# Kernel optimization log

Measured on AMD Instinct MI355X. Metric: run time of the kernel, lower is better.

Reference implementation:

```python
import math
import jax, jax.numpy as jnp
import numpy as np

N, L, C_IMG, D, FF, H, NL, V = 2, 1024, 512, 512, 2048, 8, 4, 8000
EPS_ATTN = 1e-6
EPS_LN = 1e-5


def pos_enc(position, channels):
    # position: (N, L, 1) float. channels assumed even here (256 / 512).
    num = channels // 2
    log_inc = math.log(10000.0) / (num - 1)
    inv = jnp.exp(jnp.arange(num, dtype=position.dtype) * -log_inc)
    st = position * inv.reshape(1, 1, -1)  # (N, L, num)
    return jnp.concatenate([jnp.sin(st), jnp.cos(st)], -1)


def layer_norm(x, s, b):
    m = jnp.mean(x, -1, keepdims=True)
    v = jnp.mean((x - m) ** 2, -1, keepdims=True)
    return (x - m) / jnp.sqrt(v + EPS_LN) * s + b


def causal_linear_attention(x, mask, Wq, bq, Wk, bk, Wv, bv, Wo, bo):
    # x: (N, L, D), mask: (N, L, 1)
    n, l, d = x.shape
    q = (x @ Wq + bq).reshape(n, l, H, -1)
    k = (x @ Wk + bk).reshape(n, l, H, -1)
    v = (x @ Wv + bv).reshape(n, l, H, -1)
    Q = jax.nn.elu(q) + 1.0                       # elu feature map
    K = (jax.nn.elu(k) + 1.0) * mask[:, :, :, None]
    K_cum = jnp.cumsum(K, axis=1)                 # (N, L, H, dk)
    Z = 1.0 / (jnp.einsum('nlhd,nlhd->nlh', Q, K_cum) + EPS_ATTN)
    KV = jnp.cumsum(K[..., :, None] * v[..., None, :], axis=1)  # (N, L, H, dk, dv)
    out = jnp.einsum('nlhd,nlhde->nlhe', Q, KV) * Z[..., None]
    return out.reshape(n, l, d) @ Wo + bo


def encoder_layer(x, mask, p):
    (Wq, bq, Wk, bk, Wv, bv, Wo, bo, W1, b1, W2, b2, s1, be1, s2, be2) = p
    x = x + causal_linear_attention(x, mask, Wq, bq, Wk, bk, Wv, bv, Wo, bo)
    x = layer_norm(x, s1, be1)
    y = jax.nn.gelu(x @ W1 + b1, approximate=False) @ W2 + b2
    return layer_norm(x + y, s2, be2)


def setup_inputs() -> dict:
    key = jax.random.key(0)
    ks = iter(jax.random.split(key, 64))

    def p(shape):
        return jax.random.normal(next(ks), shape, dtype=jnp.float32) * 0.02

    x_img = jax.random.normal(next(ks), (N, L, C_IMG), dtype=jnp.float32)
    x_txt = jax.random.randint(next(ks), (N, L), 0, V)
    pos = jnp.broadcast_to(jnp.arange(L, dtype=jnp.float32)[None, :, None], (N, L, 1))
    pos_r = jnp.floor(pos / 32.0)
    pos_c = jnp.mod(pos, 32.0)
    pos_t = pos
    first_half = (jnp.arange(L) < L // 2).astype(jnp.float32)[None, :, None]
    mask_img = jnp.broadcast_to(first_half, (N, L, 1))
    mask_txt = 1.0 - mask_img

    inp = dict(x_img=x_img, x_txt=x_txt, mask_img=mask_img, mask_txt=mask_txt,
               pos_r=pos_r, pos_c=pos_c, pos_t=pos_t,
               W_ei=p((C_IMG, D)), b_ei=jnp.zeros((D,)),
               emb_txt=p((V, D)),
               Wq=p((NL, D, D)), bq=jnp.zeros((NL, D)),
               Wk=p((NL, D, D)), bk=jnp.zeros((NL, D)),
               Wv=p((NL, D, D)), bv=jnp.zeros((NL, D)),
               Wo=p((NL, D, D)), bo=jnp.zeros((NL, D)),
               W1=p((NL, D, FF)), b1=jnp.zeros((NL, FF)),
               W2=p((NL, FF, D)), b2=jnp.zeros((NL, D)),
               ln1_s=jnp.ones((NL, D)), ln1_b=jnp.zeros((NL, D)),
               ln2_s=jnp.ones((NL, D)), ln2_b=jnp.zeros((NL, D)),
               W_pi=p((D, C_IMG)), b_pi=jnp.zeros((C_IMG,)),
               W_pt=p((D, V)), b_pt=jnp.zeros((V,)))
    return inp


def reference(x_img, x_txt, mask_img, mask_txt, pos_r, pos_c, pos_t,
              W_ei, b_ei, emb_txt,
              Wq, bq, Wk, bk, Wv, bv, Wo, bo, W1, b1, W2, b2,
              ln1_s, ln1_b, ln2_s, ln2_b, W_pi, b_pi, W_pt, b_pt):
    x_mask = mask_img + mask_txt  # (N, L, 1)
    # image embedding
    half = D // 2
    x_pos = jnp.concatenate([pos_enc(pos_r, half), pos_enc(pos_c, D - half)], -1)
    x_emb_img = ((x_img @ W_ei + b_ei) + x_pos) * mask_img
    # text embedding
    x_emb_txt = (emb_txt[x_txt] + pos_enc(pos_t, D)) * mask_txt
    x = x_emb_img + x_emb_txt
    for i in range(NL):
        p = (Wq[i], bq[i], Wk[i], bk[i], Wv[i], bv[i], Wo[i], bo[i],
             W1[i], b1[i], W2[i], b2[i], ln1_s[i], ln1_b[i], ln2_s[i], ln2_b[i])
        x = encoder_layer(x, x_mask, p)
    logit_img = x @ W_pi + b_pi
    logit_txt = x @ W_pt + b_pt
    return (logit_img, logit_txt)
```

## Files before the change

### kernel.cpp

```cpp
#include <hip/hip_runtime.h>
#include <hip/hip_bf16.h>
#include <math.h>

#define NB 2
#define LSEQ 1024
#define DM 512
#define FFD 2048
#define NHEAD 8
#define DKH 64
#define NLAYER 4
#define VOCAB 8000
#define NCHUNK 16
#define NROWS (NB * LSEQ)
#define QS 1536
#define NHEADCAT 8512
#define NHEADPAD 8576

#define OP_NONE 0
#define OP_GELU 2
#define OP_QKV  3
#define OP_PART 4
#define OP_HEAD 5

typedef __attribute__((ext_vector_type(8))) short short8;
typedef __attribute__((ext_vector_type(4))) float f32x4;
typedef __hip_bfloat16 bf16;

__device__ __forceinline__ void cast_tile(
    const float* __restrict__ s, bf16* __restrict__ d, int K, int N,
    int n0, int k0, int tx, int ty)
{
    __shared__ float tile[32][33];
    #pragma unroll
    for (int i = 0; i < 4; ++i) {
        const int k = k0 + ty + 8 * i;
        const int n = n0 + tx;
        tile[ty + 8 * i][tx] = (n < N) ? s[(size_t)k * N + n] : 0.f;
    }
    __syncthreads();
    #pragma unroll
    for (int i = 0; i < 4; ++i) {
        const int n = n0 + ty + 8 * i;
        d[(size_t)n * K + k0 + tx] = __float2bfloat16(tile[tx][ty + 8 * i]);
    }
}

__global__ __launch_bounds__(256) void cast_t(
    const float* __restrict__ src, bf16* __restrict__ dst,
    int K, int N, size_t sStride, size_t dStride)
{
    const int z = blockIdx.z;
    cast_tile(src + (size_t)z * sStride, dst + (size_t)z * dStride, K, N,
              blockIdx.x * 32, blockIdx.y * 32,
              threadIdx.x & 31, threadIdx.x >> 5);
}

__global__ __launch_bounds__(256) void cast_qkvo(
    const float* __restrict__ Wq, const float* __restrict__ Wk,
    const float* __restrict__ Wv, const float* __restrict__ Wo,
    bf16* __restrict__ QKVt, bf16* __restrict__ Wot)
{
    const int z = blockIdx.z, layer = z >> 2, which = z & 3;
    const float* src = (which == 0 ? Wq : which == 1 ? Wk : which == 2 ? Wv : Wo)
                       + (size_t)layer * 262144;
    bf16* dst = (which < 3) ? (QKVt + (size_t)layer * 786432 + (size_t)which * 262144)
                            : (Wot + (size_t)layer * 262144);
    cast_tile(src, dst, 512, 512, blockIdx.x * 32, blockIdx.y * 32,
              threadIdx.x & 31, threadIdx.x >> 5);
}

__global__ __launch_bounds__(256) void cast_e(
    const float* __restrict__ src, bf16* __restrict__ dst, int n4)
{
    const int i = blockIdx.x * 256 + threadIdx.x;
    if (i < n4) {
        const float4 v = *(const float4*)(src + (size_t)i * 4);
        dst[(size_t)i * 4 + 0] = __float2bfloat16(v.x);
        dst[(size_t)i * 4 + 1] = __float2bfloat16(v.y);
        dst[(size_t)i * 4 + 2] = __float2bfloat16(v.z);
        dst[(size_t)i * 4 + 3] = __float2bfloat16(v.w);
    }
}

__global__ __launch_bounds__(256) void qkv_bias_k(
    const float* __restrict__ bq, const float* __restrict__ bk,
    const float* __restrict__ bv, float* __restrict__ out)
{
    const int z = blockIdx.x;
    for (int j = threadIdx.x; j < QS; j += 256) {
        float v;
        if (j < 512)       v = bq[z * DM + j];
        else if (j < 1024) v = bk[z * DM + j - 512];
        else               v = bv[z * DM + j - 1024];
        out[z * QS + j] = v;
    }
}

__global__ __launch_bounds__(256) void head_bias_k(
    const float* __restrict__ bpi, const float* __restrict__ bpt,
    float* __restrict__ hb)
{
    const int j = blockIdx.x * 256 + threadIdx.x;
    if (j < NHEADPAD)
        hb[j] = (j < 512) ? bpi[j] : (j < NHEADCAT ? bpt[j - 512] : 0.f);
}

template<int BM, int BN>
__global__ __launch_bounds__(256) void gemm16(
    const bf16* __restrict__ A, const bf16* __restrict__ Bt,
    const float* __restrict__ bias, const float* __restrict__ res,
    float* __restrict__ outF, float* __restrict__ outF2,
    bf16* __restrict__ outH,
    int M, int K, int Nout, int op, int kslab)
{
    constexpr int WM = BM / 2, WN = BN / 2, MI = WM / 16, NI = WN / 16;
    __shared__ bf16 As[BM * 32];
    __shared__ bf16 Bs[BN * 32];
    const int tid = threadIdx.x;
    const int lane = tid & 63;
    const int wave = tid >> 6;
    const int wm = (wave >> 1) * WM, wn = (wave & 1) * WN;
    const int bm = blockIdx.y * BM, bn = blockIdx.x * BN;
    const int l16 = lane & 15, quad = lane >> 4;

    const int rA = tid >> 2;
    const int c8 = (tid & 3) << 3;

    f32x4 acc[MI][NI];
    #pragma unroll
    for (int i = 0; i < MI; ++i)
        #pragma unroll
        for (int j = 0; j < NI; ++j) acc[i][j] = (f32x4){0.f, 0.f, 0.f, 0.f};

    const bf16* gA = A  + (size_t)(bm + rA) * K + c8;
    const bf16* gB = Bt + (size_t)(bn + rA) * K + c8;
    const int ldsWaveOff = wave * 1024;

    const int kStart = blockIdx.z * kslab;
    for (int k0 = kStart; k0 < kStart + kslab; k0 += 32) {
        __syncthreads();
        #pragma unroll
        for (int i = 0; i < BM / 64; ++i)
            __builtin_amdgcn_global_load_lds(
                (const __attribute__((address_space(1))) void*)(gA + (size_t)i * 64 * K + k0),
                (__attribute__((address_space(3))) void*)((char*)As + i * 4096 + ldsWaveOff),
                16, 0, 0);
        #pragma unroll
        for (int i = 0; i < BN / 64; ++i)
            __builtin_amdgcn_global_load_lds(
                (const __attribute__((address_space(1))) void*)(gB + (size_t)i * 64 * K + k0),
                (__attribute__((address_space(3))) void*)((char*)Bs + i * 4096 + ldsWaveOff),
                16, 0, 0);
        __syncthreads();
        short8 a[MI], b[NI];
        #pragma unroll
        for (int i = 0; i < MI; ++i)
            a[i] = *(const short8*)(As + (size_t)(wm + i * 16 + l16) * 32 + quad * 8);
        #pragma unroll
        for (int j = 0; j < NI; ++j)
            b[j] = *(const short8*)(Bs + (size_t)(wn + j * 16 + l16) * 32 + quad * 8);
        #pragma unroll
        for (int i = 0; i < MI; ++i)
            #pragma unroll
            for (int j = 0; j < NI; ++j)
                acc[i][j] = __builtin_amdgcn_mfma_f32_16x16x32_bf16(
                    a[i], b[j], acc[i][j], 0, 0, 0);
    }

    if (op == OP_PART) {
        float* dst = outF + (size_t)blockIdx.z * (size_t)M * Nout;
        #pragma unroll
        for (int j = 0; j < NI; ++j) {
            const int col = bn + wn + j * 16 + l16;
            #pragma unroll
            for (int i = 0; i < MI; ++i)
                #pragma unroll
                for (int r = 0; r < 4; ++r) {
                    const int row = bm + wm + i * 16 + quad * 4 + r;
                    dst[(size_t)row * Nout + col] = acc[i][j][r];
                }
        }
        return;
    }
    if (op == OP_HEAD) {
        #pragma unroll
        for (int j = 0; j < NI; ++j) {
            const int col = bn + wn + j * 16 + l16;
            const bool cok = (col < NHEADCAT);
            const float bz = cok ? bias[col] : 0.f;
            #pragma unroll
            for (int i = 0; i < MI; ++i)
                #pragma unroll
                for (int r = 0; r < 4; ++r) {
                    const int row = bm + wm + i * 16 + quad * 4 + r;
                    const float v = acc[i][j][r] + bz;
                    if (cok) {
                        if (col < 512) outF[(size_t)row * 512 + col] = v;
                        else           outF2[(size_t)row * VOCAB + (col - 512)] = v;
                    }
                }
        }
        return;
    }

    #pragma unroll
    for (int j = 0; j < NI; ++j) {
        const int col = bn + wn + j * 16 + l16;
        const bool cok = (col < Nout);
        const float bz = cok ? bias[col] : 0.f;
        #pragma unroll
        for (int i = 0; i < MI; ++i) {
            #pragma unroll
            for (int r = 0; r < 4; ++r) {
                const int row = bm + wm + i * 16 + quad * 4 + r;
                float v = acc[i][j][r] + bz;
                if (op == OP_GELU)      v = 0.5f * v * (1.f + erff(v * 0.70710678118654752f));
                else if (op == OP_QKV && col < 1024) v = (v > 0.f) ? v + 1.f : expf(v);
                if (cok) {
                    if (res)  v += res[(size_t)row * Nout + col];
                    if (outF) outF[(size_t)row * Nout + col] = v;
                    if (outH) outH[(size_t)row * Nout + col] = __float2bfloat16(v);
                }
            }
        }
    }
}

__global__ __launch_bounds__(256) void embed_k(
    const float* __restrict__ gI, const int* __restrict__ xt,
    const float* __restrict__ emb,
    const float* __restrict__ mi, const float* __restrict__ mt,
    const float* __restrict__ pr, const float* __restrict__ pc,
    const float* __restrict__ pt, float* __restrict__ X, bf16* __restrict__ Xh)
{
    const int row = blockIdx.x;
    const float prv = pr[row], pcv = pc[row], ptv = pt[row];
    const float miv = mi[row], mtv = mt[row];
    const int tok = xt[row];
    const float LOG1E4 = 9.2103403719761836f;
    const float LI127 = LOG1E4 / 127.f;
    const float LI255 = LOG1E4 / 255.f;

    for (int d = threadIdx.x; d < DM; d += 256) {
        float ip;
        if (d < 128)       ip = sinf(prv * expf(-(float)d * LI127));
        else if (d < 256)  ip = cosf(prv * expf(-(float)(d - 128) * LI127));
        else if (d < 384)  ip = sinf(pcv * expf(-(float)(d - 256) * LI127));
        else               ip = cosf(pcv * expf(-(float)(d - 384) * LI127));
        float tp;
        if (d < 256) tp = sinf(ptv * expf(-(float)d * LI255));
        else         tp = cosf(ptv * expf(-(float)(d - 256) * LI255));
        const float v = miv * (gI[(size_t)row * DM + d] + ip)
                      + mtv * (emb[(size_t)tok * DM + d] + tp);
        X[(size_t)row * DM + d] = v;
        Xh[(size_t)row * DM + d] = __float2bfloat16(v);
    }
}

__global__ __launch_bounds__(256) void ln_red(
    const float* __restrict__ P, int nP,
    const float* __restrict__ bias, const float* __restrict__ res,
    const float* __restrict__ g, const float* __restrict__ b,
    float* __restrict__ out, bf16* __restrict__ outh)
{
    const int row = blockIdx.x;
    const int tid = threadIdx.x;
    const size_t base = (size_t)row * DM;
    float x0 = res[base + tid] + bias[tid];
    float x1 = res[base + tid + 256] + bias[tid + 256];
    for (int p = 0; p < nP; ++p) {
        x0 += P[(size_t)p * 1048576 + base + tid];
        x1 += P[(size_t)p * 1048576 + base + tid + 256];
    }
    __shared__ float red[256];
    red[tid] = x0 + x1;
    __syncthreads();
    for (int off = 128; off > 0; off >>= 1) {
        if (tid < off) red[tid] += red[tid + off];
        __syncthreads();
    }
    const float mean = red[0] / (float)DM;
    __syncthreads();
    const float d0 = x0 - mean, d1 = x1 - mean;
    red[tid] = d0 * d0 + d1 * d1;
    __syncthreads();
    for (int off = 128; off > 0; off >>= 1) {
        if (tid < off) red[tid] += red[tid + off];
        __syncthreads();
    }
    const float var = red[0] / (float)DM;
    const float rstd = rsqrtf(var + 1e-5f);
    const float y0 = d0 * rstd * g[tid] + b[tid];
    const float y1 = d1 * rstd * g[tid + 256] + b[tid + 256];
    out[base + tid]        = y0;
    out[base + tid + 256]  = y1;
    outh[base + tid]       = __float2bfloat16(y0);
    outh[base + tid + 256] = __float2bfloat16(y1);
}

__global__ __launch_bounds__(256) void attn_kv(
    const float* __restrict__ Kp, const float* __restrict__ Vp,
    float* __restrict__ S, float* __restrict__ ks)
{
    const int c = blockIdx.x, h = blockIdx.y, n = blockIdx.z;
    const int tid = threadIdx.x;
    __shared__ float sK[64][64], sV[64][64], part[4][64];

    const int lr = tid >> 4;
    const int c4 = (tid & 15) * 4;
    #pragma unroll
    for (int it = 0; it < 4; ++it) {
        const int row = it * 16 + lr;
        const size_t gb = ((size_t)(n * LSEQ + c * 64 + row)) * QS + h * DKH + c4;
        *(float4*)&sK[row][c4] = *(const float4*)(Kp + gb);
        *(float4*)&sV[row][c4] = *(const float4*)(Vp + gb);
    }
    __syncthreads();

    const int e = tid & 63, dq = tid >> 6;
    float s[16] = {};
    for (int l = 0; l < 64; ++l) {
        const float vv = sV[l][e];
        const float4 k0 = *(const float4*)&sK[l][dq * 16 + 0];
        const float4 k1 = *(const float4*)&sK[l][dq * 16 + 4];
        const float4 k2 = *(const float4*)&sK[l][dq * 16 + 8];
        const float4 k3 = *(const float4*)&sK[l][dq * 16 + 12];
        s[0]  = fmaf(k0.x, vv, s[0]);  s[1]  = fmaf(k0.y, vv, s[1]);
        s[2]  = fmaf(k0.z, vv, s[2]);  s[3]  = fmaf(k0.w, vv, s[3]);
        s[4]  = fmaf(k1.x, vv, s[4]);  s[5]  = fmaf(k1.y, vv, s[5]);
        s[6]  = fmaf(k1.z, vv, s[6]);  s[7]  = fmaf(k1.w, vv, s[7]);
        s[8]  = fmaf(k2.x, vv, s[8]);  s[9]  = fmaf(k2.y, vv, s[9]);
        s[10] = fmaf(k2.z, vv, s[10]); s[11] = fmaf(k2.w, vv, s[11]);
        s[12] = fmaf(k3.x, vv, s[12]); s[13] = fmaf(k3.y, vv, s[13]);
        s[14] = fmaf(k3.z, vv, s[14]); s[15] = fmaf(k3.w, vv, s[15]);
    }
    const size_t sb = (((size_t)(n * NHEAD + h)) * NCHUNK + c) * 4096;
    #pragma unroll
    for (int i = 0; i < 16; ++i) S[sb + (size_t)(dq * 16 + i) * 64 + e] = s[i];

    float kp = 0.f;
    #pragma unroll
    for (int i = 0; i < 16; ++i) kp += sK[dq * 16 + i][e];
    part[dq][e] = kp;
    __syncthreads();
    if (tid < 64)
        ks[(((size_t)(n * NHEAD + h)) * NCHUNK + c) * 64 + tid] =
            part[0][tid] + part[1][tid] + part[2][tid] + part[3][tid];
}

__global__ __launch_bounds__(256) void attn_prefix(
    float* __restrict__ S, float* __restrict__ ks)
{
    const int gid = blockIdx.x * 256 + threadIdx.x;
    const int nh = gid >> 12, j = gid & 4095;
    const size_t base = ((size_t)nh * NCHUNK) * 4096 + j;
    float run = 0.f;
    #pragma unroll
    for (int c = 0; c < NCHUNK; ++c) {
        const float t = S[base + (size_t)c * 4096];
        S[base + (size_t)c * 4096] = run;
        run += t;
    }
    if (gid < NB * NHEAD * 64) {
        const int nh2 = gid >> 6, j2 = gid & 63;
        const size_t kb = ((size_t)nh2 * NCHUNK) * 64 + j2;
        float kr = 0.f;
        #pragma unroll
        for (int c = 0; c < NCHUNK; ++c) {
            const float t = ks[kb + c * 64];
            ks[kb + c * 64] = kr;
            kr += t;
        }
    }
}

__global__ __launch_bounds__(256) void attn_out(
    const float* __restrict__ QKV, const float* __restrict__ S,
    const float* __restrict__ ks, bf16* __restrict__ O)
{
    const int c = blockIdx.x, h = blockIdx.y, n = blockIdx.z;
    const int tid = threadIdx.x;
    __shared__ float sQt[64][64];
    __shared__ float sKt[64][64];
    __shared__ float sV [64][64];
    __shared__ float sS [64][64];
    __shared__ float sPt[64][65];
    __shared__ float skp[64];

    const int lr = tid >> 4;
    const int c4 = (tid & 15) * 4;
    const size_t sb = (((size_t)(n * NHEAD + h)) * NCHUNK + c) * 4096;
    #pragma unroll
    for (int it = 0; it < 4; ++it) {
        const int row = it * 16 + lr;
        const size_t gb = ((size_t)(n * LSEQ + c * 64 + row)) * QS + h * DKH + c4;
        const float4 q4 = *(const float4*)(QKV + gb);
        const float4 k4 = *(const float4*)(QKV + gb + 512);
        const float4 v4 = *(const float4*)(QKV + gb + 1024);
        sQt[c4 + 0][row] = q4.x; sQt[c4 + 1][row] = q4.y;
        sQt[c4 + 2][row] = q4.z; sQt[c4 + 3][row] = q4.w;
        sKt[c4 + 0][row] = k4.x; sKt[c4 + 1][row] = k4.y;
        sKt[c4 + 2][row] = k4.z; sKt[c4 + 3][row] = k4.w;
        *(float4*)&sV[row][c4] = v4;
        *(float4*)&sS[row][c4] = *(const float4*)(S + sb + (size_t)row * 64 + c4);
    }
    if (tid < 64) skp[tid] = ks[(((size_t)(n * NHEAD + h)) * NCHUNK + c) * 64 + tid];
    __syncthreads();

    const int m4 = (tid & 15) * 4;
    const int lg = tid >> 4;
    {
        float p[4][4] = {};
        for (int d = 0; d < 64; ++d) {
            const float4 k4 = *(const float4*)&sKt[d][m4];
            const float4 q4 = *(const float4*)&sQt[d][lg * 4];
            p[0][0] = fmaf(q4.x, k4.x, p[0][0]); p[0][1] = fmaf(q4.x, k4.y, p[0][1]);
            p[0][2] = fmaf(q4.x, k4.z, p[0][2]); p[0][3] = fmaf(q4.x, k4.w, p[0][3]);
            p[1][0] = fmaf(q4.y, k4.x, p[1][0]); p[1][1] = fmaf(q4.y, k4.y, p[1][1]);
            p[1][2] = fmaf(q4.y, k4.z, p[1][2]); p[1][3] = fmaf(q4.y, k4.w, p[1][3]);
            p[2][0] = fmaf(q4.z, k4.x, p[2][0]); p[2][1] = fmaf(q4.z, k4.y, p[2][1]);
            p[2][2] = fmaf(q4.z, k4.z, p[2][2]); p[2][3] = fmaf(q4.z, k4.w, p[2][3]);
            p[3][0] = fmaf(q4.w, k4.x, p[3][0]); p[3][1] = fmaf(q4.w, k4.y, p[3][1]);
            p[3][2] = fmaf(q4.w, k4.z, p[3][2]); p[3][3] = fmaf(q4.w, k4.w, p[3][3]);
        }
        #pragma unroll
        for (int jj = 0; jj < 4; ++jj)
            #pragma unroll
            for (int j = 0; j < 4; ++j)
                sPt[m4 + jj][lg * 4 + j] = p[j][jj];
    }
    __syncthreads();

    float acc[4][4] = {};
    float z[4] = {};
    const int lmax = lg * 4 + 3;
    for (int m = 0; m <= lmax; ++m) {
        const float4 v4 = *(const float4*)&sV[m][m4];
        #pragma unroll
        for (int j = 0; j < 4; ++j) {
            const int l = lg * 4 + j;
            float p = sPt[m][l];
            p = (m <= l) ? p : 0.f;
            z[j] += p;
            acc[j][0] = fmaf(p, v4.x, acc[j][0]);
            acc[j][1] = fmaf(p, v4.y, acc[j][1]);
            acc[j][2] = fmaf(p, v4.z, acc[j][2]);
            acc[j][3] = fmaf(p, v4.w, acc[j][3]);
        }
    }
    for (int d = 0; d < 64; ++d) {
        const float4 s4 = *(const float4*)&sS[d][m4];
        const float4 q4 = *(const float4*)&sQt[d][lg * 4];
        const float kp = skp[d];
        z[0] = fmaf(q4.x, kp, z[0]); z[1] = fmaf(q4.y, kp, z[1]);
        z[2] = fmaf(q4.z, kp, z[2]); z[3] = fmaf(q4.w, kp, z[3]);
        acc[0][0] = fmaf(q4.x, s4.x, acc[0][0]); acc[0][1] = fmaf(q4.x, s4.y, acc[0][1]);
        acc[0][2] = fmaf(q4.x, s4.z, acc[0][2]); acc[0][3] = fmaf(q4.x, s4.w, acc[0][3]);
        acc[1][0] = fmaf(q4.y, s4.x, acc[1][0]); acc[1][1] = fmaf(q4.y, s4.y, acc[1][1]);
        acc[1][2] = fmaf(q4.y, s4.z, acc[1][2]); acc[1][3] = fmaf(q4.y, s4.w, acc[1][3]);
        acc[2][0] = fmaf(q4.z, s4.x, acc[2][0]); acc[2][1] = fmaf(q4.z, s4.y, acc[2][1]);
        acc[2][2] = fmaf(q4.z, s4.z, acc[2][2]); acc[2][3] = fmaf(q4.z, s4.w, acc[2][3]);
        acc[3][0] = fmaf(q4.w, s4.x, acc[3][0]); acc[3][1] = fmaf(q4.w, s4.y, acc[3][1]);
        acc[3][2] = fmaf(q4.w, s4.z, acc[3][2]); acc[3][3] = fmaf(q4.w, s4.w, acc[3][3]);
    }
    #pragma unroll
    for (int j = 0; j < 4; ++j) {
        const int l = lg * 4 + j;
        const float rz = 1.f / (z[j] + 1e-6f);
        const size_t ob = ((size_t)(n * LSEQ + c * 64 + l)) * DM + h * DKH + m4;
        O[ob + 0] = __float2bfloat16(acc[j][0] * rz);
        O[ob + 1] = __float2bfloat16(acc[j][1] * rz);
        O[ob + 2] = __float2bfloat16(acc[j][2] * rz);
        O[ob + 3] = __float2bfloat16(acc[j][3] * rz);
    }
}

extern "C" void kernel_launch(void* const* d_in, const int* in_sizes, int n_in,
                              void* d_out, int out_size, void* d_ws, size_t ws_size,
                              hipStream_t stream)
{
    const float* x_img   = (const float*)d_in[0];
    const int*   x_txt   = (const int*)  d_in[1];
    const float* mask_i  = (const float*)d_in[2];
    const float* mask_t  = (const float*)d_in[3];
    const float* pos_r   = (const float*)d_in[4];
    const float* pos_c   = (const float*)d_in[5];
    const float* pos_t   = (const float*)d_in[6];
    const float* W_ei    = (const float*)d_in[7];
    const float* b_ei    = (const float*)d_in[8];
    const float* emb_txt = (const float*)d_in[9];
    const float* Wq      = (const float*)d_in[10];
    const float* bq      = (const float*)d_in[11];
    const float* Wk      = (const float*)d_in[12];
    const float* bk      = (const float*)d_in[13];
    const float* Wv      = (const float*)d_in[14];
    const float* bv      = (const float*)d_in[15];
    const float* Wo      = (const float*)d_in[16];
    const float* bo      = (const float*)d_in[17];
    const float* W1      = (const float*)d_in[18];
    const float* b1      = (const float*)d_in[19];
    const float* W2      = (const float*)d_in[20];
    const float* b2      = (const float*)d_in[21];
    const float* ln1_s   = (const float*)d_in[22];
    const float* ln1_b   = (const float*)d_in[23];
    const float* ln2_s   = (const float*)d_in[24];
    const float* ln2_b   = (const float*)d_in[25];
    const float* W_pi    = (const float*)d_in[26];
    const float* b_pi    = (const float*)d_in[27];
    const float* W_pt    = (const float*)d_in[28];
    const float* b_pt    = (const float*)d_in[29];

    float* ws = (float*)d_ws;
    size_t off = 0;
    auto alloc = [&](size_t nfloats) { float* p = ws + off; off += nfloats; return p; };

    float* Xb   = alloc(1048576);
    float* Pb   = alloc(4194304);
    float* QKVb = alloc(3145728);
    float* Sb   = alloc(1048576);
    float* ksb  = alloc(16384);
    float* qkvB = alloc(4 * QS);
    float* hb   = alloc(8704);
    bf16* Xh    = (bf16*)alloc(524288);
    bf16* Ob    = (bf16*)alloc(524288);
    bf16* Tb    = (bf16*)alloc(2097152);
    bf16* ximgh = (bf16*)alloc(524288);
    bf16* QKVt  = (bf16*)alloc(1572864);
    bf16* Wot   = (bf16*)alloc(524288);
    bf16* W1t   = (bf16*)alloc(2097152);
    bf16* W2t   = (bf16*)alloc(2097152);
    bf16* Weit  = (bf16*)alloc(131072);
    bf16* Whead = (bf16*)alloc(2195456);

    const dim3 blk(256);
    const dim3 gAttn(NCHUNK, NHEAD, NB);

    cast_qkvo<<<dim3(16, 16, 16), blk, 0, stream>>>(Wq, Wk, Wv, Wo, QKVt, Wot);
    cast_t<<<dim3(64, 16, 4), blk, 0, stream>>>(W1, W1t, 512, 2048, 1048576, 1048576);
    cast_t<<<dim3(16, 64, 4), blk, 0, stream>>>(W2, W2t, 2048, 512, 1048576, 1048576);
    cast_t<<<dim3(16, 16, 1), blk, 0, stream>>>(W_ei, Weit, 512, 512, 0, 0);
    cast_t<<<dim3(16, 16, 1), blk, 0, stream>>>(W_pi, Whead, 512, 512, 0, 0);
    cast_t<<<dim3(252, 16, 1), blk, 0, stream>>>(W_pt, Whead + 262144, 512, VOCAB, 0, 0);
    cast_e<<<dim3(1024), blk, 0, stream>>>(x_img, ximgh, 262144);
    qkv_bias_k<<<dim3(4), blk, 0, stream>>>(bq, bk, bv, qkvB);
    head_bias_k<<<dim3(34), blk, 0, stream>>>(b_pi, b_pt, hb);

    gemm16<64, 64><<<dim3(8, 32), blk, 0, stream>>>(
        ximgh, Weit, b_ei, nullptr, Pb, nullptr, nullptr, NROWS, 512, 512, OP_NONE, 512);
    embed_k<<<NROWS, blk, 0, stream>>>(Pb, x_txt, emb_txt, mask_i, mask_t,
                                       pos_r, pos_c, pos_t, Xb, Xh);

    for (int i = 0; i < NLAYER; ++i) {
        gemm16<64, 128><<<dim3(12, 32), blk, 0, stream>>>(
            Xh, QKVt + (size_t)i * 786432, qkvB + i * QS, nullptr,
            QKVb, nullptr, nullptr, NROWS, 512, QS, OP_QKV, 512);

        attn_kv<<<gAttn, blk, 0, stream>>>(QKVb + 512, QKVb + 1024, Sb, ksb);
        attn_prefix<<<dim3(256), blk, 0, stream>>>(Sb, ksb);
        attn_out<<<gAttn, blk, 0, stream>>>(QKVb, Sb, ksb, Ob);

        gemm16<64, 64><<<dim3(8, 32, 2), blk, 0, stream>>>(
            Ob, Wot + (size_t)i * 262144, nullptr, nullptr,
            Pb, nullptr, nullptr, NROWS, 512, 512, OP_PART, 256);
        ln_red<<<NROWS, blk, 0, stream>>>(Pb, 2, bo + (size_t)i * DM, Xb,
                                          ln1_s + (size_t)i * DM,
                                          ln1_b + (size_t)i * DM, Xb, Xh);

        gemm16<128, 128><<<dim3(16, 16), blk, 0, stream>>>(
            Xh, W1t + (size_t)i * 1048576, b1 + (size_t)i * FFD, nullptr,
            nullptr, nullptr, Tb, NROWS, 512, FFD, OP_GELU, 512);
        gemm16<64, 64><<<dim3(8, 32, 4), blk, 0, stream>>>(
            Tb, W2t + (size_t)i * 1048576, nullptr, nullptr,
            Pb, nullptr, nullptr, NROWS, 2048, 512, OP_PART, 512);
        ln_red<<<NROWS, blk, 0, stream>>>(Pb, 4, b2 + (size_t)i * DM, Xb,
                                          ln2_s + (size_t)i * DM,
                                          ln2_b + (size_t)i * DM, Xb, Xh);
    }

    float* out = (float*)d_out;
    gemm16<128, 128><<<dim3(67, 16), blk, 0, stream>>>(
        Xh, Whead, hb, nullptr, out, out + 1048576, nullptr,
        NROWS, 512, NHEADCAT, OP_HEAD, 512);
}
```

Baseline: 702.8 us.

## Merge setup casts into one kernel, fold chunk prefix into attn_out, retile FFN1

```diff
diff --git a/kernel.cpp b/kernel.cpp
--- a/kernel.cpp
+++ b/kernel.cpp
@@ -45,64 +45,87 @@
     }
 }
 
-__global__ __launch_bounds__(256) void cast_t(
-    const float* __restrict__ src, bf16* __restrict__ dst,
-    int K, int N, size_t sStride, size_t dStride)
-{
-    const int z = blockIdx.z;
-    cast_tile(src + (size_t)z * sStride, dst + (size_t)z * dStride, K, N,
-              blockIdx.x * 32, blockIdx.y * 32,
-              threadIdx.x & 31, threadIdx.x >> 5);
-}
-
-__global__ __launch_bounds__(256) void cast_qkvo(
+#define CO_QKVO 0
+#define CO_W1   4096
+#define CO_W2   8192
+#define CO_WEI  12288
+#define CO_WPI  12544
+#define CO_WPT  12800
+#define CO_XIMG 16832
+#define CO_QKVB 17856
+#define CO_HB   17860
+#define CO_END  17894
+
+__global__ __launch_bounds__(256) void setup_all(
     const float* __restrict__ Wq, const float* __restrict__ Wk,
     const float* __restrict__ Wv, const float* __restrict__ Wo,
-    bf16* __restrict__ QKVt, bf16* __restrict__ Wot)
-{
-    const int z = blockIdx.z, layer = z >> 2, which = z & 3;
-    const float* src = (which == 0 ? Wq : which == 1 ? Wk : which == 2 ? Wv : Wo)
-                       + (size_t)layer * 262144;
-    bf16* dst = (which < 3) ? (QKVt + (size_t)layer * 786432 + (size_t)which * 262144)
-                            : (Wot + (size_t)layer * 262144);
-    cast_tile(src, dst, 512, 512, blockIdx.x * 32, blockIdx.y * 32,
-              threadIdx.x & 31, threadIdx.x >> 5);
-}
-
-__global__ __launch_bounds__(256) void cast_e(
-    const float* __restrict__ src, bf16* __restrict__ dst, int n4)
-{
-    const int i = blockIdx.x * 256 + threadIdx.x;
-    if (i < n4) {
-        const float4 v = *(const float4*)(src + (size_t)i * 4);
-        dst[(size_t)i * 4 + 0] = __float2bfloat16(v.x);
-        dst[(size_t)i * 4 + 1] = __float2bfloat16(v.y);
-        dst[(size_t)i * 4 + 2] = __float2bfloat16(v.z);
-        dst[(size_t)i * 4 + 3] = __float2bfloat16(v.w);
-    }
-}
-
-__global__ __launch_bounds__(256) void qkv_bias_k(
+    const float* __restrict__ W1, const float* __restrict__ W2,
+    const float* __restrict__ Wei, const float* __restrict__ Wpi,
+    const float* __restrict__ Wpt,
+    bf16* __restrict__ QKVt, bf16* __restrict__ Wot,
+    bf16* __restrict__ W1t, bf16* __restrict__ W2t,
+    bf16* __restrict__ Weit, bf16* __restrict__ Whead,
+    const float* __restrict__ x_img, bf16* __restrict__ ximgh,
     const float* __restrict__ bq, const float* __restrict__ bk,
-    const float* __restrict__ bv, float* __restrict__ out)
-{
-    const int z = blockIdx.x;
-    for (int j = threadIdx.x; j < QS; j += 256) {
-        float v;
-        if (j < 512)       v = bq[z * DM + j];
-        else if (j < 1024) v = bk[z * DM + j - 512];
-        else               v = bv[z * DM + j - 1024];
-        out[z * QS + j] = v;
-    }
-}
-
-__global__ __launch_bounds__(256) void head_bias_k(
+    const float* __restrict__ bv, float* __restrict__ qkvB,
     const float* __restrict__ bpi, const float* __restrict__ bpt,
     float* __restrict__ hb)
 {
-    const int j = blockIdx.x * 256 + threadIdx.x;
-    if (j < NHEADPAD)
-        hb[j] = (j < 512) ? bpi[j] : (j < NHEADCAT ? bpt[j - 512] : 0.f);
+    const int id = blockIdx.x;
+    const int tid = threadIdx.x;
+    const int tx = tid & 31, ty = tid >> 5;
+
+    if (id < CO_W1) {
+        const int rel = id;
+        const int z = rel >> 8, t = rel & 255;
+        const int layer = z >> 2, which = z & 3;
+        const float* src = (which == 0 ? Wq : which == 1 ? Wk : which == 2 ? Wv : Wo)
+                           + (size_t)layer * 262144;
+        bf16* dst = (which < 3)
+            ? (QKVt + (size_t)layer * 786432 + (size_t)which * 262144)
+            : (Wot + (size_t)layer * 262144);
+        cast_tile(src, dst, 512, 512, (t & 15) * 32, (t >> 4) * 32, tx, ty);
+    } else if (id < CO_W2) {
+        const int rel = id - CO_W1;
+        const int z = rel >> 10, t = rel & 1023;
+        cast_tile(W1 + (size_t)z * 1048576, W1t + (size_t)z * 1048576,
+                  512, 2048, (t & 63) * 32, (t >> 6) * 32, tx, ty);
+    } else if (id < CO_WEI) {
+        const int rel = id - CO_W2;
+        const int z = rel >> 10, t = rel & 1023;
+        cast_tile(W2 + (size_t)z * 1048576, W2t + (size_t)z * 1048576,
+                  2048, 512, (t & 15) * 32, (t >> 4) * 32, tx, ty);
+    } else if (id < CO_WPI) {
+        const int t = id - CO_WEI;
+        cast_tile(Wei, Weit, 512, 512, (t & 15) * 32, (t >> 4) * 32, tx, ty);
+    } else if (id < CO_WPT) {
+        const int t = id - CO_WPI;
+        cast_tile(Wpi, Whead, 512, 512, (t & 15) * 32, (t >> 4) * 32, tx, ty);
+    } else if (id < CO_XIMG) {
+        const int t = id - CO_WPT;
+        cast_tile(Wpt, Whead + 262144, 512, VOCAB,
+                  (t % 252) * 32, (t / 252) * 32, tx, ty);
+    } else if (id < CO_QKVB) {
+        const int i = (id - CO_XIMG) * 256 + tid;
+        const float4 v = *(const float4*)(x_img + (size_t)i * 4);
+        ximgh[(size_t)i * 4 + 0] = __float2bfloat16(v.x);
+        ximgh[(size_t)i * 4 + 1] = __float2bfloat16(v.y);
+        ximgh[(size_t)i * 4 + 2] = __float2bfloat16(v.z);
+        ximgh[(size_t)i * 4 + 3] = __float2bfloat16(v.w);
+    } else if (id < CO_HB) {
+        const int z = id - CO_QKVB;
+        for (int j = tid; j < QS; j += 256) {
+            float v;
+            if (j < 512)       v = bq[z * DM + j];
+            else if (j < 1024) v = bk[z * DM + j - 512];
+            else               v = bv[z * DM + j - 1024];
+            qkvB[z * QS + j] = v;
+        }
+    } else {
+        const int j = (id - CO_HB) * 256 + tid;
+        if (j < NHEADPAD)
+            hb[j] = (j < 512) ? bpi[j] : (j < NHEADCAT ? bpt[j - 512] : 0.f);
+    }
 }
 
 template<int BM, int BN>
@@ -120,7 +143,8 @@
     const int lane = tid & 63;
     const int wave = tid >> 6;
     const int wm = (wave >> 1) * WM, wn = (wave & 1) * WN;
-    const int bm = blockIdx.y * BM, bn = blockIdx.x * BN;
+    const int bm = (op == OP_HEAD ? blockIdx.x : blockIdx.y) * BM;
+    const int bn = (op == OP_HEAD ? blockIdx.y : blockIdx.x) * BN;
     const int l16 = lane & 15, quad = lane >> 4;
 
     const int rA = tid >> 2;
@@ -348,32 +372,6 @@
             part[0][tid] + part[1][tid] + part[2][tid] + part[3][tid];
 }
 
-__global__ __launch_bounds__(256) void attn_prefix(
-    float* __restrict__ S, float* __restrict__ ks)
-{
-    const int gid = blockIdx.x * 256 + threadIdx.x;
-    const int nh = gid >> 12, j = gid & 4095;
-    const size_t base = ((size_t)nh * NCHUNK) * 4096 + j;
-    float run = 0.f;
-    #pragma unroll
-    for (int c = 0; c < NCHUNK; ++c) {
-        const float t = S[base + (size_t)c * 4096];
-        S[base + (size_t)c * 4096] = run;
-        run += t;
-    }
-    if (gid < NB * NHEAD * 64) {
-        const int nh2 = gid >> 6, j2 = gid & 63;
-        const size_t kb = ((size_t)nh2 * NCHUNK) * 64 + j2;
-        float kr = 0.f;
-        #pragma unroll
-        for (int c = 0; c < NCHUNK; ++c) {
-            const float t = ks[kb + c * 64];
-            ks[kb + c * 64] = kr;
-            kr += t;
-        }
-    }
-}
-
 __global__ __launch_bounds__(256) void attn_out(
     const float* __restrict__ QKV, const float* __restrict__ S,
     const float* __restrict__ ks, bf16* __restrict__ O)
@@ -387,9 +385,32 @@
     __shared__ float sPt[64][65];
     __shared__ float skp[64];
 
+    const size_t nhS = ((size_t)(n * NHEAD + h)) * NCHUNK * 4096;
+    const size_t nhK = ((size_t)(n * NHEAD + h)) * NCHUNK * 64;
+
+    {
+        float4 aS[4] = {};
+        for (int cc = 0; cc < c; ++cc) {
+            const float* Sc = S + nhS + (size_t)cc * 4096;
+            #pragma unroll
+            for (int i = 0; i < 4; ++i) {
+                const float4 t = *(const float4*)(Sc + i * 1024 + tid * 4);
+                aS[i].x += t.x; aS[i].y += t.y; aS[i].z += t.z; aS[i].w += t.w;
+            }
+        }
+        float* sSf = &sS[0][0];
+        #pragma unroll
+        for (int i = 0; i < 4; ++i)
+            *(float4*)(sSf + i * 1024 + tid * 4) = aS[i];
+        if (tid < 64) {
+            float kp = 0.f;
+            for (int cc = 0; cc < c; ++cc) kp += ks[nhK + cc * 64 + tid];
+            skp[tid] = kp;
+        }
+    }
+
     const int lr = tid >> 4;
     const int c4 = (tid & 15) * 4;
-    const size_t sb = (((size_t)(n * NHEAD + h)) * NCHUNK + c) * 4096;
     #pragma unroll
     for (int it = 0; it < 4; ++it) {
         const int row = it * 16 + lr;
@@ -402,9 +423,7 @@
         sKt[c4 + 0][row] = k4.x; sKt[c4 + 1][row] = k4.y;
         sKt[c4 + 2][row] = k4.z; sKt[c4 + 3][row] = k4.w;
         *(float4*)&sV[row][c4] = v4;
-        *(float4*)&sS[row][c4] = *(const float4*)(S + sb + (size_t)row * 64 + c4);
-    }
-    if (tid < 64) skp[tid] = ks[(((size_t)(n * NHEAD + h)) * NCHUNK + c) * 64 + tid];
+    }
     __syncthreads();
 
     const int m4 = (tid & 15) * 4;
@@ -535,15 +554,10 @@
     const dim3 blk(256);
     const dim3 gAttn(NCHUNK, NHEAD, NB);
 
-    cast_qkvo<<<dim3(16, 16, 16), blk, 0, stream>>>(Wq, Wk, Wv, Wo, QKVt, Wot);
-    cast_t<<<dim3(64, 16, 4), blk, 0, stream>>>(W1, W1t, 512, 2048, 1048576, 1048576);
-    cast_t<<<dim3(16, 64, 4), blk, 0, stream>>>(W2, W2t, 2048, 512, 1048576, 1048576);
-    cast_t<<<dim3(16, 16, 1), blk, 0, stream>>>(W_ei, Weit, 512, 512, 0, 0);
-    cast_t<<<dim3(16, 16, 1), blk, 0, stream>>>(W_pi, Whead, 512, 512, 0, 0);
-    cast_t<<<dim3(252, 16, 1), blk, 0, stream>>>(W_pt, Whead + 262144, 512, VOCAB, 0, 0);
-    cast_e<<<dim3(1024), blk, 0, stream>>>(x_img, ximgh, 262144);
-    qkv_bias_k<<<dim3(4), blk, 0, stream>>>(bq, bk, bv, qkvB);
-    head_bias_k<<<dim3(34), blk, 0, stream>>>(b_pi, b_pt, hb);
+    setup_all<<<dim3(CO_END), blk, 0, stream>>>(
+        Wq, Wk, Wv, Wo, W1, W2, W_ei, W_pi, W_pt,
+        QKVt, Wot, W1t, W2t, Weit, Whead,
+        x_img, ximgh, bq, bk, bv, qkvB, b_pi, b_pt, hb);
 
     gemm16<64, 64><<<dim3(8, 32), blk, 0, stream>>>(
         ximgh, Weit, b_ei, nullptr, Pb, nullptr, nullptr, NROWS, 512, 512, OP_NONE, 512);
@@ -556,7 +570,6 @@
             QKVb, nullptr, nullptr, NROWS, 512, QS, OP_QKV, 512);
 
         attn_kv<<<gAttn, blk, 0, stream>>>(QKVb + 512, QKVb + 1024, Sb, ksb);
-        attn_prefix<<<dim3(256), blk, 0, stream>>>(Sb, ksb);
         attn_out<<<gAttn, blk, 0, stream>>>(QKVb, Sb, ksb, Ob);
 
         gemm16<64, 64><<<dim3(8, 32, 2), blk, 0, stream>>>(
@@ -566,7 +579,7 @@
                                           ln1_s + (size_t)i * DM,
                                           ln1_b + (size_t)i * DM, Xb, Xh);
 
-        gemm16<128, 128><<<dim3(16, 16), blk, 0, stream>>>(
+        gemm16<64, 128><<<dim3(16, 32), blk, 0, stream>>>(
             Xh, W1t + (size_t)i * 1048576, b1 + (size_t)i * FFD, nullptr,
             nullptr, nullptr, Tb, NROWS, 512, FFD, OP_GELU, 512);
         gemm16<64, 64><<<dim3(8, 32, 4), blk, 0, stream>>>(
@@ -578,7 +591,7 @@
     }
 
     float* out = (float*)d_out;
-    gemm16<128, 128><<<dim3(67, 16), blk, 0, stream>>>(
+    gemm16<128, 128><<<dim3(16, 67), blk, 0, stream>>>(
         Xh, Whead, hb, nullptr, out, out + 1048576, nullptr,
         NROWS, 512, NHEADCAT, OP_HEAD, 512);
 }
```

After: 650.9 us. -7.4%, faster.
